# Performance work log

Measured on AMD Instinct MI355X. Metric: run time of the kernel, lower is better.

## Reference

```python
import jax, jax.numpy as jnp
from jax import lax
import numpy as np

IN_C, OUT_C, K, N_SPLIT = 256, 256, 3, 4
N_LEGO = int(OUT_C * 0.25)          # 64
BASIC_C = IN_C // N_SPLIT           # 64


def setup_inputs() -> dict:
    key = jax.random.key(0)
    k1, k2, k3, k4 = jax.random.split(key, 4)
    x = jax.random.normal(k1, (32, IN_C, 56, 56), dtype=jnp.float32)
    # kaiming-normal-ish initialization of parameters
    lego = jax.random.normal(k2, (N_LEGO, BASIC_C, K, 1), dtype=jnp.float32) * np.sqrt(2.0 / (BASIC_C * K))
    aux_coefficients = jax.random.normal(k3, (N_SPLIT, OUT_C, N_LEGO, 1, 1), dtype=jnp.float32) * np.sqrt(2.0 / N_LEGO)
    aux_combination = jax.random.normal(k4, (N_SPLIT, OUT_C, N_LEGO, 1, 1), dtype=jnp.float32) * np.sqrt(2.0 / N_LEGO)
    return {"x": x, "lego": lego, "aux_coefficients": aux_coefficients, "aux_combination": aux_combination}


def reference(x, lego, aux_coefficients, aux_combination):
    n_split, out_c, n_lego = aux_combination.shape[:3]
    bc = lego.shape[1]
    # one-hot selection: each (split, out_channel) picks exactly one lego feature
    idx = jnp.argmax(aux_combination[..., 0, 0], axis=2)              # (n_split, out_c)
    proxy = jax.nn.one_hot(idx, n_lego, dtype=x.dtype)                # (n_split, out_c, n_lego)
    W = aux_coefficients[..., 0, 0] * proxy                           # (n_split, out_c, n_lego)
    out = 0.0
    for i in range(n_split):
        xi = x[:, i * bc:(i + 1) * bc]                                # (B, bc, H, W)
        feat = lax.conv_general_dilated(
            xi, lego, window_strides=(3, 1), padding=((1, 1), (1, 1)),
            dimension_numbers=("NCHW", "OIHW", "NCHW"))               # (B, n_lego, Ho, Wo)
        out = out + jnp.einsum("bnhw,on->bohw", feat, W[i])
    return out
```

## Files before the change

kernel.cpp:

```cpp
#include <hip/hip_runtime.h>

#define INC    256
#define HIN    56
#define WIN    56
#define HOUT   19
#define WOUT   58
#define KTOT   768

typedef short frag8 __attribute__((ext_vector_type(8)));
typedef float f32x4 __attribute__((ext_vector_type(4)));

static __device__ __forceinline__ unsigned short f2bf(float f) {
    unsigned u = __float_as_uint(f);
    u += 0x7fffu + ((u >> 16) & 1u);
    return (unsigned short)(u >> 16);
}

__global__ __launch_bounds__(256) void prep_weff(
    const float* __restrict__ lego,
    const float* __restrict__ coefs,
    const float* __restrict__ comb,
    unsigned short* __restrict__ Asw)
{
    __shared__ int   idxS[4];
    __shared__ float cofS[4];
    const int t  = threadIdx.x;
    const int kx = blockIdx.x;
    const int o  = blockIdx.y;
    const int wv = t >> 6, l = t & 63;

    float v  = comb[(wv * 256 + o) * 64 + l];
    int   bi = l;
    #pragma unroll
    for (int off = 32; off >= 1; off >>= 1) {
        float ov = __shfl_xor(v, off, 64);
        int   oi = __shfl_xor(bi, off, 64);
        if (ov > v || (ov == v && oi < bi)) { v = ov; bi = oi; }
    }
    if (l == 0) {
        idxS[wv] = bi;
        cofS[wv] = coefs[(wv * 256 + o) * 64 + bi];
    }
    __syncthreads();

    const int k  = kx * 256 + t;
    const int kh = k >> 8, c = k & 255;
    const int i  = c >> 6, cl = c & 63;
    float w = cofS[i] * lego[idxS[i] * 192 + cl * 3 + kh];

    const int o_tile = o >> 4, m = o & 15;
    const int ks = k >> 5, kc = (k >> 3) & 3, j = k & 7;
    Asw[((((size_t)o_tile * 24 + ks) * 64) + kc * 16 + m) * 8 + j] = f2bf(w);
}

__global__ __launch_bounds__(256, 5) void conv_mfma(
    const float* __restrict__ x,
    const unsigned short* __restrict__ Asw,
    float* __restrict__ out)
{
    __shared__ unsigned short Xs[12 * 2 * 64 * 8];

    const int t  = threadIdx.x;
    const int wh = blockIdx.x;
    const int h  = blockIdx.y;
    const int b  = blockIdx.z;

    const int l  = t & 63;
    const int lo = l & 15;
    const int hi = l >> 4;
    const int wv = t >> 6;

    f32x4 acc[4][2];
    #pragma unroll
    for (int ot = 0; ot < 4; ++ot)
        #pragma unroll
        for (int nt = 0; nt < 2; ++nt)
            acc[ot][nt] = (f32x4){0.f, 0.f, 0.f, 0.f};

    const float* xb = x + (size_t)b * (INC * HIN * WIN);
    const int w     = t & 31;
    const int kg    = t >> 5;
    const int col   = wh * 32 - 1 + w;
    const bool colok = (unsigned)col < (unsigned)WIN;
    const int wtile = w >> 4;
    const int lbase = w & 15;
    const int rowbase = 3 * h - 1;

    const frag8* Af = (const frag8*)Asw + ((size_t)(wv * 4) * 24) * 64 + l;
    const frag8* Xf = (const frag8*)Xs + l;

    for (int c2 = 0; c2 < 2; ++c2) {
        #pragma unroll
        for (int q = 0; q < 6; ++q) {
            int p   = kg * 6 + q;
            int ksl = p >> 2, kc = p & 3;
            int kgl = c2 * 384 + ksl * 32 + kc * 8;
            int kh  = kgl >> 8, c0 = kgl & 255;
            int row = rowbase + kh;
            bool ok = colok && ((unsigned)row < (unsigned)HIN);
            const float* xp = xb + (size_t)c0 * (HIN * WIN) + row * WIN + col;
            union { frag8 f; unsigned short u[8]; } pk;
            #pragma unroll
            for (int j = 0; j < 8; ++j) {
                float v = ok ? xp[(size_t)j * (HIN * WIN)] : 0.f;
                pk.u[j] = f2bf(v);
            }
            *(frag8*)&Xs[(((ksl * 2 + wtile) * 64) + kc * 16 + lbase) * 8] = pk.f;
        }
        __syncthreads();

        const int ksb = c2 * 12;
        frag8 a[4], an[4], b0, b1, b0n, b1n;
        #pragma unroll
        for (int ot = 0; ot < 4; ++ot) a[ot] = Af[(ot * 24 + ksb) * 64];
        b0 = Xf[0];
        b1 = Xf[64];

        #pragma unroll
        for (int ks = 0; ks < 11; ++ks) {
            #pragma unroll
            for (int ot = 0; ot < 4; ++ot) an[ot] = Af[(ot * 24 + ksb + ks + 1) * 64];
            b0n = Xf[((ks + 1) * 2) * 64];
            b1n = Xf[((ks + 1) * 2 + 1) * 64];

            #pragma unroll
            for (int ot = 0; ot < 4; ++ot) {
                acc[ot][0] = __builtin_amdgcn_mfma_f32_16x16x32_bf16(a[ot], b0, acc[ot][0], 0, 0, 0);
                acc[ot][1] = __builtin_amdgcn_mfma_f32_16x16x32_bf16(a[ot], b1, acc[ot][1], 0, 0, 0);
            }
            #pragma unroll
            for (int ot = 0; ot < 4; ++ot) a[ot] = an[ot];
            b0 = b0n; b1 = b1n;
        }
        #pragma unroll
        for (int ot = 0; ot < 4; ++ot) {
            acc[ot][0] = __builtin_amdgcn_mfma_f32_16x16x32_bf16(a[ot], b0, acc[ot][0], 0, 0, 0);
            acc[ot][1] = __builtin_amdgcn_mfma_f32_16x16x32_bf16(a[ot], b1, acc[ot][1], 0, 0, 0);
        }
        __syncthreads();
    }

    const int wb = wh * 32;
    const int obase = wv * 64;
    #pragma unroll
    for (int ot = 0; ot < 4; ++ot) {
        #pragma unroll
        for (int nt = 0; nt < 2; ++nt) {
            int wcol = wb + nt * 16 + lo;
            if (wcol < WOUT) {
                #pragma unroll
                for (int r = 0; r < 4; ++r) {
                    int o = obase + ot * 16 + hi * 4 + r;
                    out[((size_t)(b * 256 + o) * HOUT + h) * WOUT + wcol] = acc[ot][nt][r];
                }
            }
        }
    }
}

extern "C" void kernel_launch(void* const* d_in, const int* in_sizes, int n_in,
                              void* d_out, int out_size, void* d_ws, size_t ws_size,
                              hipStream_t stream) {
    const float* x     = (const float*)d_in[0];
    const float* lego  = (const float*)d_in[1];
    const float* coefs = (const float*)d_in[2];
    const float* comb  = (const float*)d_in[3];
    float* out = (float*)d_out;

    unsigned short* Asw = (unsigned short*)d_ws;

    prep_weff<<<dim3(3, 256), 256, 0, stream>>>(lego, coefs, comb, Asw);
    conv_mfma<<<dim3(2, HOUT, 32), 256, 0, stream>>>(x, Asw, out);
}
```

Baseline: 193.1 us.

## Double-buffer LDS input tiles per kernel row with vectorized float4 loads

Restructures the conv input staging into three per-kh chunks (256 channels each) held in a double-buffered LDS tile, so global loads for the next row overlap the MFMA work on the current one. Each thread now loads float4 spans of four columns across eight channels instead of scalar loads, and LDS writes and reads use an XOR swizzle to avoid bank conflicts. The occupancy hint drops from 5 to 4 blocks per SM because the extra buffer raises register and LDS use. Unaligned float4 loads and the extra barriers are the risks.

```diff
diff --git a/kernel.cpp b/kernel.cpp
--- a/kernel.cpp
+++ b/kernel.cpp
@@ -9,6 +9,8 @@
 
 typedef short frag8 __attribute__((ext_vector_type(8)));
 typedef float f32x4 __attribute__((ext_vector_type(4)));
+typedef float f4    __attribute__((ext_vector_type(4)));
+typedef f4 f4a __attribute__((aligned(4)));
 
 static __device__ __forceinline__ unsigned short f2bf(float f) {
     unsigned u = __float_as_uint(f);
@@ -53,12 +55,76 @@
     Asw[((((size_t)o_tile * 24 + ks) * 64) + kc * 16 + m) * 8 + j] = f2bf(w);
 }
 
-__global__ __launch_bounds__(256, 5) void conv_mfma(
+
+static __device__ __forceinline__ void load_rows(
+    const float* __restrict__ xr,
+    bool rok, int col4, f4 v[8])
+{
+    const size_t HW = (size_t)HIN * WIN;
+    const bool allok = rok && (col4 >= 0) && (col4 + 3 < WIN);
+    if (allok) {
+        #pragma unroll
+        for (int j = 0; j < 8; ++j)
+            v[j] = *(const f4a*)(xr + j * HW);
+    } else {
+        #pragma unroll
+        for (int j = 0; j < 8; ++j) {
+            #pragma unroll
+            for (int e = 0; e < 4; ++e) {
+                int c = col4 + e;
+                v[j][e] = (rok && (unsigned)c < (unsigned)WIN) ? xr[j * HW + e] : 0.f;
+            }
+        }
+    }
+}
+
+static __device__ __forceinline__ void write_chunk(
+    unsigned short* __restrict__ bsb,
+    int kc, const f4 v[8])
+{
+    #pragma unroll
+    for (int i = 0; i < 4; ++i) {
+        union { frag8 f; unsigned short u[8]; } pk;
+        #pragma unroll
+        for (int j = 0; j < 8; ++j) pk.u[j] = f2bf(v[j][i]);
+        *(frag8*)(bsb + (i ^ kc) * 8) = pk.f;
+    }
+}
+
+static __device__ __forceinline__ void mfma_chunk(
+    const frag8* __restrict__ Af,
+    const frag8* __restrict__ Xf,
+    int ksb, f32x4 (&acc)[4][2])
+{
+    frag8 a[4], an[4];
+    #pragma unroll
+    for (int ot = 0; ot < 4; ++ot) a[ot] = Af[(ot * 24 + ksb) * 64];
+    #pragma unroll
+    for (int ks = 0; ks < 8; ++ks) {
+        if (ks < 7) {
+            #pragma unroll
+            for (int ot = 0; ot < 4; ++ot) an[ot] = Af[(ot * 24 + ksb + ks + 1) * 64];
+        }
+        frag8 b0 = Xf[(ks * 2) * 64];
+        frag8 b1 = Xf[(ks * 2 + 1) * 64];
+        #pragma unroll
+        for (int ot = 0; ot < 4; ++ot) {
+            acc[ot][0] = __builtin_amdgcn_mfma_f32_16x16x32_bf16(a[ot], b0, acc[ot][0], 0, 0, 0);
+            acc[ot][1] = __builtin_amdgcn_mfma_f32_16x16x32_bf16(a[ot], b1, acc[ot][1], 0, 0, 0);
+        }
+        if (ks < 7) {
+            #pragma unroll
+            for (int ot = 0; ot < 4; ++ot) a[ot] = an[ot];
+        }
+    }
+}
+
+__global__ __launch_bounds__(256, 4) void conv_mfma(
     const float* __restrict__ x,
     const unsigned short* __restrict__ Asw,
     float* __restrict__ out)
 {
-    __shared__ unsigned short Xs[12 * 2 * 64 * 8];
+    __shared__ unsigned short Xs[2][8 * 2 * 64 * 8];
 
     const int t  = threadIdx.x;
     const int wh = blockIdx.x;
@@ -77,68 +143,39 @@
         for (int nt = 0; nt < 2; ++nt)
             acc[ot][nt] = (f32x4){0.f, 0.f, 0.f, 0.f};
 
-    const float* xb = x + (size_t)b * (INC * HIN * WIN);
-    const int w     = t & 31;
-    const int kg    = t >> 5;
-    const int col   = wh * 32 - 1 + w;
-    const bool colok = (unsigned)col < (unsigned)WIN;
-    const int wtile = w >> 4;
-    const int lbase = w & 15;
+    const int cg   = t & 7;
+    const int pg   = t >> 3;
+    const int chb  = pg * 8;
+    const int col4 = wh * 32 - 1 + cg * 4;
     const int rowbase = 3 * h - 1;
+    const size_t HW = (size_t)HIN * WIN;
+    const float* xpt = x + (size_t)b * (INC * HIN * WIN) + (size_t)chb * HW;
+
+    const int ksl = pg >> 2, kc = pg & 3, wt = cg >> 2, lb = (cg & 3) * 4;
+    const int wslot = (((ksl * 2 + wt) * 64) + kc * 16 + lb) * 8;
 
     const frag8* Af = (const frag8*)Asw + ((size_t)(wv * 4) * 24) * 64 + l;
-    const frag8* Xf = (const frag8*)Xs + l;
-
-    for (int c2 = 0; c2 < 2; ++c2) {
-        #pragma unroll
-        for (int q = 0; q < 6; ++q) {
-            int p   = kg * 6 + q;
-            int ksl = p >> 2, kc = p & 3;
-            int kgl = c2 * 384 + ksl * 32 + kc * 8;
-            int kh  = kgl >> 8, c0 = kgl & 255;
-            int row = rowbase + kh;
-            bool ok = colok && ((unsigned)row < (unsigned)HIN);
-            const float* xp = xb + (size_t)c0 * (HIN * WIN) + row * WIN + col;
-            union { frag8 f; unsigned short u[8]; } pk;
-            #pragma unroll
-            for (int j = 0; j < 8; ++j) {
-                float v = ok ? xp[(size_t)j * (HIN * WIN)] : 0.f;
-                pk.u[j] = f2bf(v);
-            }
-            *(frag8*)&Xs[(((ksl * 2 + wtile) * 64) + kc * 16 + lbase) * 8] = pk.f;
-        }
-        __syncthreads();
-
-        const int ksb = c2 * 12;
-        frag8 a[4], an[4], b0, b1, b0n, b1n;
-        #pragma unroll
-        for (int ot = 0; ot < 4; ++ot) a[ot] = Af[(ot * 24 + ksb) * 64];
-        b0 = Xf[0];
-        b1 = Xf[64];
-
-        #pragma unroll
-        for (int ks = 0; ks < 11; ++ks) {
-            #pragma unroll
-            for (int ot = 0; ot < 4; ++ot) an[ot] = Af[(ot * 24 + ksb + ks + 1) * 64];
-            b0n = Xf[((ks + 1) * 2) * 64];
-            b1n = Xf[((ks + 1) * 2 + 1) * 64];
-
-            #pragma unroll
-            for (int ot = 0; ot < 4; ++ot) {
-                acc[ot][0] = __builtin_amdgcn_mfma_f32_16x16x32_bf16(a[ot], b0, acc[ot][0], 0, 0, 0);
-                acc[ot][1] = __builtin_amdgcn_mfma_f32_16x16x32_bf16(a[ot], b1, acc[ot][1], 0, 0, 0);
-            }
-            #pragma unroll
-            for (int ot = 0; ot < 4; ++ot) a[ot] = an[ot];
-            b0 = b0n; b1 = b1n;
-        }
-        #pragma unroll
-        for (int ot = 0; ot < 4; ++ot) {
-            acc[ot][0] = __builtin_amdgcn_mfma_f32_16x16x32_bf16(a[ot], b0, acc[ot][0], 0, 0, 0);
-            acc[ot][1] = __builtin_amdgcn_mfma_f32_16x16x32_bf16(a[ot], b1, acc[ot][1], 0, 0, 0);
-        }
-        __syncthreads();
-    }
+    const int xfo = l ^ (l >> 4);
+    const frag8* Xf0 = (const frag8*)Xs[0] + xfo;
+    const frag8* Xf1 = (const frag8*)Xs[1] + xfo;
+
+    f4 v[8];
+
+    load_rows(xpt + (ptrdiff_t)rowbase * WIN + col4, (unsigned)rowbase < (unsigned)HIN, col4, v);
+    write_chunk(&Xs[0][wslot], kc, v);
+    load_rows(xpt + (ptrdiff_t)(rowbase + 1) * WIN + col4, (unsigned)(rowbase + 1) < (unsigned)HIN, col4, v);
+    __syncthreads();
+
+    mfma_chunk(Af, Xf0, 0, acc);
+    write_chunk(&Xs[1][wslot], kc, v);
+    load_rows(xpt + (ptrdiff_t)(rowbase + 2) * WIN + col4, (unsigned)(rowbase + 2) < (unsigned)HIN, col4, v);
+    __syncthreads();
+
+    mfma_chunk(Af, Xf1, 8, acc);
+    write_chunk(&Xs[0][wslot], kc, v);
+    __syncthreads();
+
+    mfma_chunk(Af, Xf0, 16, acc);
 
     const int wb = wh * 32;
     const int obase = wv * 64;
```

After: 214.7 us. 1.11x slower.

## Stream fp32 input rows into LDS with async triple-buffered global_load_lds pipeline

Applied to the files above, without the earlier changes.

Rewrites the conv kernel so each block covers a full output row (64 columns) with a 12-stage K loop. Input rows are copied asynchronously as fp32 via global_load_lds into a 3-deep LDS ring with swizzled slots, and converted to bf16 at fragment-build time with v_cvt_pk_bf16_f32. Padding columns are written as explicit zeros instead of being computed. This aims to overlap global loads with MFMA work and to remove per-thread scalar loads and conversion before staging. In exchange it uses more LDS, lowers the occupancy target to 3, and relies on hand-placed vmcnt waits and barriers.

```diff
diff --git a/kernel.cpp b/kernel.cpp
--- a/kernel.cpp
+++ b/kernel.cpp
@@ -5,16 +5,26 @@
 #define WIN    56
 #define HOUT   19
 #define WOUT   58
-#define KTOT   768
+#define HW     3136
 
 typedef short frag8 __attribute__((ext_vector_type(8)));
 typedef float f32x4 __attribute__((ext_vector_type(4)));
+typedef float f4    __attribute__((ext_vector_type(4)));
 
 static __device__ __forceinline__ unsigned short f2bf(float f) {
     unsigned u = __float_as_uint(f);
     u += 0x7fffu + ((u >> 16) & 1u);
     return (unsigned short)(u >> 16);
 }
+
+static __device__ __forceinline__ unsigned cvtpk(float a, float b) {
+    unsigned r;
+    asm("v_cvt_pk_bf16_f32 %0, %1, %2" : "=v"(r) : "v"(a), "v"(b));
+    return r;
+}
+
+#define VMCNT(n) asm volatile("s_waitcnt vmcnt(" #n ")" ::: "memory")
+#define FENCE()  asm volatile("" ::: "memory")
 
 __global__ __launch_bounds__(256) void prep_weff(
     const float* __restrict__ lego,
@@ -53,107 +63,141 @@
     Asw[((((size_t)o_tile * 24 + ks) * 64) + kc * 16 + m) * 8 + j] = f2bf(w);
 }
 
-__global__ __launch_bounds__(256, 5) void conv_mfma(
+__global__ __launch_bounds__(256, 3) void conv_mfma(
     const float* __restrict__ x,
     const unsigned short* __restrict__ Asw,
     float* __restrict__ out)
 {
-    __shared__ unsigned short Xs[12 * 2 * 64 * 8];
+    __shared__ float Xs[3][4096];
 
     const int t  = threadIdx.x;
-    const int wh = blockIdx.x;
-    const int h  = blockIdx.y;
-    const int b  = blockIdx.z;
-
+    const int h  = blockIdx.x;
+    const int b  = blockIdx.y;
     const int l  = t & 63;
     const int lo = l & 15;
     const int hi = l >> 4;
     const int wv = t >> 6;
-
-    f32x4 acc[4][2];
+    const int kc = hi;
+
+    int slotb[4];
+    #pragma unroll
+    for (int wt = 0; wt < 4; ++wt) {
+        int c    = wt * 16 + lo;
+        int slot = (c & 32) | ((c + 8 * kc) & 31);
+        slotb[wt] = slot * 4;
+    }
+    const int bko = kc * 2048;
+
+    const int gs = l & 15, chof = l >> 4;
+    unsigned goff[4];
+    int      ldsu[4];
+    #pragma unroll
+    for (int i = 0; i < 4; ++i) {
+        int I    = wv * 4 + i;
+        int chl  = I * 4 + chof;
+        int kcs  = (chl >> 3) & 3;
+        int half = gs >> 3, gsw = gs & 7;
+        int g    = (gsw - 2 * kcs) & 7;
+        int col  = half * 32 + g * 4;
+        if (col >= WIN) col = 0;
+        goff[i] = (unsigned)chl * HW + col;
+        ldsu[i] = I * 1024;
+    }
+
+    const float* xb = x + (size_t)b * (INC * HW);
+    const frag8* Af = (const frag8*)Asw + (size_t)(wv * 4) * 24 * 64 + l;
+    char* XsB = (char*)&Xs[0][0];
+
+    f32x4 acc[4][4];
     #pragma unroll
     for (int ot = 0; ot < 4; ++ot)
         #pragma unroll
-        for (int nt = 0; nt < 2; ++nt)
-            acc[ot][nt] = (f32x4){0.f, 0.f, 0.f, 0.f};
-
-    const float* xb = x + (size_t)b * (INC * HIN * WIN);
-    const int w     = t & 31;
-    const int kg    = t >> 5;
-    const int col   = wh * 32 - 1 + w;
-    const bool colok = (unsigned)col < (unsigned)WIN;
-    const int wtile = w >> 4;
-    const int lbase = w & 15;
-    const int rowbase = 3 * h - 1;
-
-    const frag8* Af = (const frag8*)Asw + ((size_t)(wv * 4) * 24) * 64 + l;
-    const frag8* Xf = (const frag8*)Xs + l;
-
-    for (int c2 = 0; c2 < 2; ++c2) {
-        #pragma unroll
-        for (int q = 0; q < 6; ++q) {
-            int p   = kg * 6 + q;
-            int ksl = p >> 2, kc = p & 3;
-            int kgl = c2 * 384 + ksl * 32 + kc * 8;
-            int kh  = kgl >> 8, c0 = kgl & 255;
-            int row = rowbase + kh;
-            bool ok = colok && ((unsigned)row < (unsigned)HIN);
-            const float* xp = xb + (size_t)c0 * (HIN * WIN) + row * WIN + col;
-            union { frag8 f; unsigned short u[8]; } pk;
-            #pragma unroll
-            for (int j = 0; j < 8; ++j) {
-                float v = ok ? xp[(size_t)j * (HIN * WIN)] : 0.f;
-                pk.u[j] = f2bf(v);
+        for (int wt = 0; wt < 4; ++wt)
+            acc[ot][wt] = (f32x4){0.f, 0.f, 0.f, 0.f};
+
+    auto STAGE = [&](int q) {
+        const int kh = q >> 2, cq = q & 3;
+        const int row = 3 * h - 1 + kh;
+        const int bufo = (q % 3) * 16384;
+        if (row < 0) {
+            f4 z = (f4){0.f, 0.f, 0.f, 0.f};
+            #pragma unroll
+            for (int i = 0; i < 4; ++i)
+                *(f4*)(XsB + bufo + ldsu[i] + l * 16) = z;
+            asm volatile("s_waitcnt lgkmcnt(0)" ::: "memory");
+        } else {
+            const float* rp = xb + (size_t)cq * 64 * HW + row * WIN;
+            #pragma unroll
+            for (int i = 0; i < 4; ++i) {
+                __builtin_amdgcn_global_load_lds(
+                    (const __attribute__((address_space(1))) void*)(rp + goff[i]),
+                    (__attribute__((address_space(3))) void*)(XsB + bufo + ldsu[i]),
+                    16, 0, 0);
             }
-            *(frag8*)&Xs[(((ksl * 2 + wtile) * 64) + kc * 16 + lbase) * 8] = pk.f;
         }
-        __syncthreads();
-
-        const int ksb = c2 * 12;
-        frag8 a[4], an[4], b0, b1, b0n, b1n;
-        #pragma unroll
-        for (int ot = 0; ot < 4; ++ot) a[ot] = Af[(ot * 24 + ksb) * 64];
-        b0 = Xf[0];
-        b1 = Xf[64];
-
-        #pragma unroll
-        for (int ks = 0; ks < 11; ++ks) {
-            #pragma unroll
-            for (int ot = 0; ot < 4; ++ot) an[ot] = Af[(ot * 24 + ksb + ks + 1) * 64];
-            b0n = Xf[((ks + 1) * 2) * 64];
-            b1n = Xf[((ks + 1) * 2 + 1) * 64];
-
-            #pragma unroll
-            for (int ot = 0; ot < 4; ++ot) {
-                acc[ot][0] = __builtin_amdgcn_mfma_f32_16x16x32_bf16(a[ot], b0, acc[ot][0], 0, 0, 0);
-                acc[ot][1] = __builtin_amdgcn_mfma_f32_16x16x32_bf16(a[ot], b1, acc[ot][1], 0, 0, 0);
+    };
+
+    STAGE(0);
+    STAGE(1);
+
+    #pragma unroll
+    for (int q = 0; q < 12; ++q) {
+        if (q + 2 < 12) STAGE(q + 2);
+
+        frag8 a[4][2];
+        #pragma unroll
+        for (int ot = 0; ot < 4; ++ot)
+            #pragma unroll
+            for (int ksl = 0; ksl < 2; ++ksl)
+                a[ot][ksl] = Af[(ot * 24 + q * 2 + ksl) * 64];
+
+        if (q < 10)       { VMCNT(16); }
+        else if (q == 10) { VMCNT(12); }
+        else              { VMCNT(8);  }
+        __builtin_amdgcn_s_barrier();
+        FENCE();
+
+        const char* bb = XsB + (q % 3) * 16384 + bko;
+        #pragma unroll
+        for (int ksl = 0; ksl < 2; ++ksl) {
+            #pragma unroll
+            for (int wt = 0; wt < 4; ++wt) {
+                float f0 = *(const float*)(bb + ksl * 8192 + 0 * 256 + slotb[wt]);
+                float f1 = *(const float*)(bb + ksl * 8192 + 1 * 256 + slotb[wt]);
+                float f2 = *(const float*)(bb + ksl * 8192 + 2 * 256 + slotb[wt]);
+                float f3 = *(const float*)(bb + ksl * 8192 + 3 * 256 + slotb[wt]);
+                float f4_ = *(const float*)(bb + ksl * 8192 + 4 * 256 + slotb[wt]);
+                float f5 = *(const float*)(bb + ksl * 8192 + 5 * 256 + slotb[wt]);
+                float f6 = *(const float*)(bb + ksl * 8192 + 6 * 256 + slotb[wt]);
+                float f7 = *(const float*)(bb + ksl * 8192 + 7 * 256 + slotb[wt]);
+                union { frag8 fr; unsigned u[4]; } B;
+                B.u[0] = cvtpk(f0, f1);
+                B.u[1] = cvtpk(f2, f3);
+                B.u[2] = cvtpk(f4_, f5);
+                B.u[3] = cvtpk(f6, f7);
+                #pragma unroll
+                for (int ot = 0; ot < 4; ++ot)
+                    acc[ot][wt] = __builtin_amdgcn_mfma_f32_16x16x32_bf16(
+                        a[ot][ksl], B.fr, acc[ot][wt], 0, 0, 0);
             }
-            #pragma unroll
-            for (int ot = 0; ot < 4; ++ot) a[ot] = an[ot];
-            b0 = b0n; b1 = b1n;
         }
-        #pragma unroll
-        for (int ot = 0; ot < 4; ++ot) {
-            acc[ot][0] = __builtin_amdgcn_mfma_f32_16x16x32_bf16(a[ot], b0, acc[ot][0], 0, 0, 0);
-            acc[ot][1] = __builtin_amdgcn_mfma_f32_16x16x32_bf16(a[ot], b1, acc[ot][1], 0, 0, 0);
-        }
-        __syncthreads();
-    }
-
-    const int wb = wh * 32;
-    const int obase = wv * 64;
+        FENCE();
+        __builtin_amdgcn_s_barrier();
+    }
+
     #pragma unroll
     for (int ot = 0; ot < 4; ++ot) {
         #pragma unroll
-        for (int nt = 0; nt < 2; ++nt) {
-            int wcol = wb + nt * 16 + lo;
-            if (wcol < WOUT) {
-                #pragma unroll
-                for (int r = 0; r < 4; ++r) {
-                    int o = obase + ot * 16 + hi * 4 + r;
-                    out[((size_t)(b * 256 + o) * HOUT + h) * WOUT + wcol] = acc[ot][nt][r];
-                }
+        for (int r = 0; r < 4; ++r) {
+            int o = wv * 64 + ot * 16 + hi * 4 + r;
+            float* orow = out + ((size_t)(b * 256 + o) * HOUT + h) * WOUT;
+            #pragma unroll
+            for (int wt = 0; wt < 4; ++wt) {
+                int n = wt * 16 + lo;
+                if (n < 56) orow[n + 1] = acc[ot][wt][r];
             }
+            if (lo == 0) orow[0]  = 0.f;
+            if (lo == 1) orow[57] = 0.f;
         }
     }
 }
@@ -170,5 +214,5 @@
     unsigned short* Asw = (unsigned short*)d_ws;
 
     prep_weff<<<dim3(3, 256), 256, 0, stream>>>(lego, coefs, comb, Asw);
-    conv_mfma<<<dim3(2, HOUT, 32), 256, 0, stream>>>(x, Asw, out);
-}
+    conv_mfma<<<dim3(HOUT, 32), 256, 0, stream>>>(x, Asw, out);
+}
```

After: 193.8 us. Within noise of the previous version (+0.4%).
